# Optimization experiments

Hardware: AMD Instinct MI355X
Metric: run time of the kernel (lower is better)

The kernel has to match this reference:

```python
import jax, jax.numpy as jnp
import numpy as np

N = 49104   # anchors (from hardcoded [2, 49104, 80] in source)
C = 80      # classes
K = 100     # max detections kept per class (fixed for jit-able output shapes)
SCORE_THRESH = 0.05
IOU_THRESH = 0.5


def setup_inputs() -> dict:
    key = jax.random.key(0)
    k1, k2 = jax.random.split(key)
    scores = jax.random.uniform(k1, (N, C), dtype=jnp.float32)
    # build valid xyxy boxes inside an ~800x800 image
    r = jax.random.uniform(k2, (N, 4), dtype=jnp.float32)
    x1 = r[:, 0] * 768.0
    y1 = r[:, 1] * 768.0
    w = r[:, 2] * 96.0 + 4.0
    h = r[:, 3] * 96.0 + 4.0
    boxes = jnp.stack([x1, y1, x1 + w, y1 + h], axis=1)
    return {"scores": scores, "boxes": boxes}


def _nms_all(scores, boxes):
    """Per-class greedy NMS, vectorized over classes via vmap.
    scores: [N, C], boxes: [N, 4] xyxy. Returns idxs/scs/valid each [C, K]."""
    areas = (boxes[:, 2] - boxes[:, 0]) * (boxes[:, 3] - boxes[:, 1])  # [N]

    def iou_vs_all(b, b_area):  # b: [4]
        ix1 = jnp.maximum(b[0], boxes[:, 0])
        iy1 = jnp.maximum(b[1], boxes[:, 1])
        ix2 = jnp.minimum(b[2], boxes[:, 2])
        iy2 = jnp.minimum(b[3], boxes[:, 3])
        inter = jnp.clip(ix2 - ix1, 0.0) * jnp.clip(iy2 - iy1, 0.0)
        return inter / (b_area + areas - inter + 1e-8)  # [N]

    def nms_one_class(s_c):  # s_c: [N]
        # score threshold (matches `scores > 0.05` masking in the torch loop)
        s0 = jnp.where(s_c > SCORE_THRESH, s_c, -jnp.inf)

        def step(s, _):
            idx = jnp.argmax(s)
            sc = s[idx]
            keep = jnp.isfinite(sc)  # anything left above threshold?
            ious = iou_vs_all(boxes[idx], areas[idx])
            suppress = (ious > IOU_THRESH) & keep
            s_next = jnp.where(suppress, -jnp.inf, s).at[idx].set(-jnp.inf)
            return s_next, (idx, sc, keep)

        _, (idxs, scs, keeps) = jax.lax.scan(step, s0, None, length=K)
        return idxs, scs, keeps  # each [K]

    return jax.vmap(nms_one_class)(scores.T)  # map over C classes


def reference(scores, boxes):
    idxs, scs, valids = _nms_all(scores, boxes)  # [C, K] each
    idxs = idxs.reshape(-1)                       # [C*K]
    valids = valids.reshape(-1)                   # [C*K] bool
    final_scores = jnp.where(valids, scs.reshape(-1), 0.0)        # [C*K]
    final_classes = jnp.repeat(jnp.arange(C, dtype=jnp.int32), K)  # [C*K]
    final_boxes = boxes[idxs] * valids[:, None].astype(boxes.dtype)  # [C*K, 4]
    return final_scores, final_classes, final_boxes, valids
```

## Files before the change

### kernel.cpp

```cpp
#include <hip/hip_runtime.h>
#include <math.h>
#include <stdint.h>

#define N_ANCH 49104
#define NCLS 80
#define KDET 100
#define CAP 256
#define TPB 256
#define NBINS 1024
#define NBLK 512
#define SUBCAP 16
#define THETA 0.996090f
#define QTOT (N_ANCH * NCLS / 4)
#define JMAX 16
#define PADKEY(t) ((0xFFFFFFFFull << 16) | (uint64_t)(t))

#define LIST_ELEMS ((size_t)NCLS * NBLK * SUBCAP)
#define SUBCNT_OFF (LIST_ELEMS * 8)
#define WS_NEED (SUBCNT_OFF + (size_t)NCLS * NBLK * 4)

__device__ __forceinline__ void collect_quad(int q, float4 v, int* lcnt,
                                             uint64_t* __restrict__ list, int blk) {
    const int n = q / 20;
    const int c0 = 4 * (q % 20);
    float ss[4] = {v.x, v.y, v.z, v.w};
#pragma unroll
    for (int u = 0; u < 4; u++) {
        float s = ss[u];
        if (s > THETA) {
            int c = c0 + u;
            int p = atomicAdd(&lcnt[c], 1);
            if (p < SUBCAP) {
                uint32_t bits = __float_as_uint(s);
                list[((size_t)c * NBLK + blk) * SUBCAP + p] =
                    ((uint64_t)(~bits) << 16) | (uint64_t)n;
            }
        }
    }
}

__global__ __launch_bounds__(TPB) void collect_kernel(const float* __restrict__ scores,
                                                      uint64_t* __restrict__ list,
                                                      int* __restrict__ subcnt) {
    const int blk = blockIdx.x, tid = threadIdx.x;
    __shared__ int lcnt[NCLS];
    for (int c = tid; c < NCLS; c += TPB) lcnt[c] = 0;
    __syncthreads();
    const float4* sc4 = (const float4*)scores;
    const int stride = NBLK * TPB;
    int q = blk * TPB + tid;
    for (; q + 3 * stride < QTOT; q += 4 * stride) {
        float4 v0 = sc4[q], v1 = sc4[q + stride], v2 = sc4[q + 2 * stride], v3 = sc4[q + 3 * stride];
        collect_quad(q, v0, lcnt, list, blk);
        collect_quad(q + stride, v1, lcnt, list, blk);
        collect_quad(q + 2 * stride, v2, lcnt, list, blk);
        collect_quad(q + 3 * stride, v3, lcnt, list, blk);
    }
    for (; q < QTOT; q += stride) collect_quad(q, sc4[q], lcnt, list, blk);
    __syncthreads();
    for (int c = tid; c < NCLS; c += TPB) subcnt[c * NBLK + blk] = lcnt[c];
}

struct ChunkShared {
    uint64_t keys[CAP];
    float4   rbox[CAP];
    float    ra[CAP], rs[CAP];
    uint64_t smat[CAP * (CAP / 64)];
    uint64_t lwbuf[CAP / 64];
    uint64_t s_kw[CAP / 64];
    int      s_cw[4];
    float4   kbox[KDET];
    float    kar[KDET], ksc[KDET];
};

__device__ __forceinline__ int process_chunk(ChunkShared& S, int tid, int M, int kc0,
                                             const float* __restrict__ boxes) {
    if (M <= 0) return kc0;
    const int lane = tid & 63, wid = tid >> 6;
    const uint64_t key = S.keys[tid];
    const int n = (int)(key & 0xFFFFull);
    const int nc = n < N_ANCH ? n : N_ANCH - 1;
    const float4 mybox = *(const float4*)(boxes + (size_t)nc * 4);
    int rank = 0;
#pragma unroll 8
    for (int j = 0; j < CAP; j++) rank += (S.keys[j] < key) ? 1 : 0;
    S.rbox[rank] = mybox;
    S.ra[rank] = (mybox.z - mybox.x) * (mybox.w - mybox.y);
    S.rs[rank] = __uint_as_float(~((uint32_t)(key >> 16)));
    __syncthreads();
    bool alive = (tid < M);
    if (alive && kc0 > 0) {
        float4 b = S.rbox[tid];
        float arb = S.ra[tid];
        for (int k2 = 0; k2 < kc0; k2++) {
            float4 kb = S.kbox[k2];
            float ix1 = fmaxf(kb.x, b.x), iy1 = fmaxf(kb.y, b.y);
            float ix2 = fminf(kb.z, b.z), iy2 = fminf(kb.w, b.w);
            float inter = fmaxf(ix2 - ix1, 0.0f) * fmaxf(iy2 - iy1, 0.0f);
            float iou = inter / (S.kar[k2] + arb - inter + 1e-8f);
            if (iou > 0.5f) { alive = false; break; }
        }
    }
    {
        uint64_t bal = __ballot(alive);
        if (lane == 0) S.lwbuf[wid] = bal;
    }
    __syncthreads();
    for (int p = wid; p < 10; p += 4) {
        const int vw = (int)((0x3333222110ull >> (4 * p)) & 0xF);
        const int ws = (int)((0x3210210100ull >> (4 * p)) & 0xF);
        const int i0 = vw << 6;
        if (i0 >= M) continue;
        const int i1 = min(M, i0 + 64);
        const int jj = (ws << 6) + lane;
        float4 bj = S.rbox[jj];
        float arj = S.ra[jj];
        for (int i = i0; i < i1; i++) {
            bool bit = false;
            if (jj < i) {
                float4 bi = S.rbox[i];
                float ari = S.ra[i];
                float ix1 = fmaxf(bj.x, bi.x), iy1 = fmaxf(bj.y, bi.y);
                float ix2 = fminf(bj.z, bi.z), iy2 = fminf(bj.w, bi.w);
                float inter = fmaxf(ix2 - ix1, 0.0f) * fmaxf(iy2 - iy1, 0.0f);
                float iou = inter / (arj + ari - inter + 1e-8f);
                bit = iou > 0.5f;
            }
            uint64_t bb = __ballot(bit);
            if (lane == 0) S.smat[((size_t)i << 2) + ws] = bb;
        }
    }
    __syncthreads();
    uint64_t st0 = 0, st1 = 0, st2 = 0, st3 = 0;
    if (tid < M) {
        st0 = S.smat[((size_t)tid << 2) + 0];
        if (wid >= 1) st1 = S.smat[((size_t)tid << 2) + 1];
        if (wid >= 2) st2 = S.smat[((size_t)tid << 2) + 2];
        if (wid >= 3) st3 = S.smat[((size_t)tid << 2) + 3];
    }
    bool kept = alive;
    bool converged = false;
    for (int it = 0; it < JMAX; it++) {
        uint64_t kb = __ballot(kept);
        if (lane == 0) S.s_kw[wid] = kb;
        __syncthreads();
        const uint64_t k0 = S.s_kw[0], k1 = S.s_kw[1], k2 = S.s_kw[2], k3 = S.s_kw[3];
        const bool sup = ((k0 & st0) | (k1 & st1) | (k2 & st2) | (k3 & st3)) != 0ull;
        const bool nk = alive && !sup;
        uint64_t cb = __ballot(nk != kept);
        if (lane == 0) S.s_cw[wid] = (cb != 0ull) ? 1 : 0;
        kept = nk;
        __syncthreads();
        if ((S.s_cw[0] | S.s_cw[1] | S.s_cw[2] | S.s_cw[3]) == 0) { converged = true; break; }
    }
    if (!converged) {
        if (tid == 0) {
            uint64_t lv[4] = {S.lwbuf[0], S.lwbuf[1], S.lwbuf[2], S.lwbuf[3]};
            uint64_t kw[4] = {0, 0, 0, 0};
            for (int i = 0; i < M; i++) {
                const int w = i >> 6, b = i & 63;
                if (!((lv[w] >> b) & 1ull)) continue;
                const uint64_t* row = &S.smat[(size_t)i << 2];
                uint64_t sup = kw[0] & row[0];
                if (w >= 1) sup |= kw[1] & row[1];
                if (w >= 2) sup |= kw[2] & row[2];
                if (w >= 3) sup |= kw[3] & row[3];
                if (!sup) kw[w] |= 1ull << b;
            }
            S.s_kw[0] = kw[0]; S.s_kw[1] = kw[1]; S.s_kw[2] = kw[2]; S.s_kw[3] = kw[3];
        }
        __syncthreads();
    }
    const uint64_t k0 = S.s_kw[0], k1 = S.s_kw[1], k2 = S.s_kw[2], k3 = S.s_kw[3];
    const int total = __popcll(k0) + __popcll(k1) + __popcll(k2) + __popcll(k3);
    const uint64_t mykw = (wid == 0) ? k0 : (wid == 1) ? k1 : (wid == 2) ? k2 : k3;
    if (tid < M && ((mykw >> lane) & 1ull)) {
        int rk = __popcll(mykw & ((1ull << lane) - 1ull));
        if (wid > 0) rk += __popcll(k0);
        if (wid > 1) rk += __popcll(k1);
        if (wid > 2) rk += __popcll(k2);
        const int r = kc0 + rk;
        if (r < KDET) { S.kbox[r] = S.rbox[tid]; S.kar[r] = S.ra[tid]; S.ksc[r] = S.rs[tid]; }
    }
    __syncthreads();
    return min(kc0 + total, KDET);
}

__global__ __launch_bounds__(TPB) void nms_final(const float* __restrict__ scores,
                                                 const float* __restrict__ boxes,
                                                 const uint64_t* __restrict__ list,
                                                 const int* __restrict__ subcnt,
                                                 int use_lists,
                                                 float* __restrict__ out) {
    const int c = blockIdx.x, tid = threadIdx.x;
    const int lane = tid & 63, wid = tid >> 6;
    __shared__ ChunkShared S;
    __shared__ int hist[NBINS];
    __shared__ int s_wtot[4];
    __shared__ int s_ov, s_cnt, s_lo;

    int kc = 0;
    bool fast = false;
    if (use_lists) {
        const int raw0 = subcnt[c * NBLK + tid];
        const int raw1 = subcnt[c * NBLK + TPB + tid];
        S.keys[tid] = PADKEY(tid);
        if (tid == 0) s_ov = 0;
        __syncthreads();
        if (raw0 > SUBCAP || raw1 > SUBCAP) atomicOr(&s_ov, 1);
        const int v0 = min(raw0, SUBCAP), v1 = min(raw1, SUBCAP);
        const int v = v0 + v1;
        int incl = v;
        for (int d = 1; d < 64; d <<= 1) {
            int o = __shfl_up(incl, d, 64);
            if (lane >= d) incl += o;
        }
        if (lane == 63) s_wtot[wid] = incl;
        __syncthreads();
        int woff = 0;
        for (int w = 0; w < wid; w++) woff += s_wtot[w];
        const int off = woff + incl - v;
        const int M0 = s_wtot[0] + s_wtot[1] + s_wtot[2] + s_wtot[3];
        fast = (s_ov == 0) && (M0 <= CAP);
        if (fast && v > 0) {
            const uint64_t* src0 = list + ((size_t)c * NBLK + tid) * SUBCAP;
            const uint64_t* src1 = list + ((size_t)c * NBLK + TPB + tid) * SUBCAP;
            for (int k = 0; k < v0; k++) S.keys[off + k] = src0[k];
            for (int k = 0; k < v1; k++) S.keys[off + v0 + k] = src1[k];
        }
        __syncthreads();
        if (fast) kc = process_chunk(S, tid, M0, 0, boxes);
    }
    if (kc < KDET) {
        const float hicut = fast ? THETA : 3.0e38f;
        if (!fast) kc = 0;
        for (int b = tid; b < NBINS; b += TPB) hist[b] = 0;
        __syncthreads();
        for (int n = tid; n < N_ANCH; n += TPB) {
            float s = scores[(size_t)n * NCLS + c];
            if (s > 0.05f && s <= hicut) {
                int b = (int)(s * 1024.0f);
                b = b < 0 ? 0 : (b > NBINS - 1 ? NBINS - 1 : b);
                atomicAdd(&hist[b], 1);
            }
        }
        __syncthreads();
        int hi = NBINS;
        while (hi > 0 && kc < KDET) {
            if (tid == 0) {
                int lo = hi, tot = 0;
                while (lo > 0 && tot + hist[lo - 1] <= CAP) { lo--; tot += hist[lo]; }
                if (lo == hi) lo = hi - 1;
                s_lo = lo; s_cnt = 0;
            }
            S.keys[tid] = PADKEY(tid);
            __syncthreads();
            const int lo = s_lo;
            for (int n = tid; n < N_ANCH; n += TPB) {
                float s = scores[(size_t)n * NCLS + c];
                if (s > 0.05f && s <= hicut) {
                    int b = (int)(s * 1024.0f);
                    b = b < 0 ? 0 : (b > NBINS - 1 ? NBINS - 1 : b);
                    if (b >= lo && b < hi) {
                        int p = atomicAdd(&s_cnt, 1);
                        if (p < CAP) {
                            uint32_t bits = __float_as_uint(s);
                            S.keys[p] = ((uint64_t)(~bits) << 16) | (uint64_t)n;
                        }
                    }
                }
            }
            __syncthreads();
            const int M2 = min(s_cnt, CAP);
            kc = process_chunk(S, tid, M2, kc, boxes);
            hi = lo;
        }
    }
    __syncthreads();

    float* o_sc = out;
    float* o_cl = out + NCLS * KDET;
    float* o_bx = out + 2 * NCLS * KDET;
    float* o_va = out + 6 * NCLS * KDET;
    for (int k = tid; k < KDET; k += TPB) {
        bool valid = k < kc;
        o_sc[c * KDET + k] = valid ? S.ksc[k] : 0.0f;
        o_cl[c * KDET + k] = (float)c;
        o_va[c * KDET + k] = valid ? 1.0f : 0.0f;
        float4 bo;
        if (valid) bo = S.kbox[k];
        else { bo.x = 0.0f; bo.y = 0.0f; bo.z = 0.0f; bo.w = 0.0f; }
        *(float4*)(o_bx + ((size_t)(c * KDET + k)) * 4) = bo;
    }
}

extern "C" void kernel_launch(void* const* d_in, const int* in_sizes, int n_in,
                              void* d_out, int out_size, void* d_ws, size_t ws_size,
                              hipStream_t stream) {
    const float* scores = (const float*)d_in[0];
    const float* boxes  = (const float*)d_in[1];
    float* out = (float*)d_out;

    uint64_t* list   = (uint64_t*)d_ws;
    int*      subcnt = (int*)((char*)d_ws + SUBCNT_OFF);
    const int use_lists = (ws_size >= WS_NEED) ? 1 : 0;

    if (use_lists) {
        collect_kernel<<<NBLK, TPB, 0, stream>>>(scores, list, subcnt);
    }
    nms_final<<<NCLS, TPB, 0, stream>>>(scores, boxes, list, subcnt, use_lists, out);
}
```

Measured before the change: 100.0 us.

## Fuse collect and NMS into one cooperative kernel with a grid sync

Merges the candidate-collection kernel and the per-class NMS kernel into a single cooperative launch separated by a grid-wide barrier, and halves the collection grid to 256 blocks so every block can be co-resident. This removes one kernel launch and the inter-kernel gap. The cost is that collection now runs on fewer blocks, and the grid sync plus the larger shared-memory footprint per block may limit occupancy. A non-cooperative fallback kernel runs only the histogram slow path.

After: 154.2 us. +54.2%, slower.

```diff
diff --git a/kernel.cpp b/kernel.cpp
--- a/kernel.cpp
+++ b/kernel.cpp
@@ -1,6 +1,9 @@
 #include <hip/hip_runtime.h>
+#include <hip/hip_cooperative_groups.h>
 #include <math.h>
 #include <stdint.h>
+
+namespace cg = cooperative_groups;
 
 #define N_ANCH 49104
 #define NCLS 80
@@ -8,7 +11,7 @@
 #define CAP 256
 #define TPB 256
 #define NBINS 1024
-#define NBLK 512
+#define NBLK 256
 #define SUBCAP 16
 #define THETA 0.996090f
 #define QTOT (N_ANCH * NCLS / 4)
@@ -37,28 +40,6 @@
             }
         }
     }
-}
-
-__global__ __launch_bounds__(TPB) void collect_kernel(const float* __restrict__ scores,
-                                                      uint64_t* __restrict__ list,
-                                                      int* __restrict__ subcnt) {
-    const int blk = blockIdx.x, tid = threadIdx.x;
-    __shared__ int lcnt[NCLS];
-    for (int c = tid; c < NCLS; c += TPB) lcnt[c] = 0;
-    __syncthreads();
-    const float4* sc4 = (const float4*)scores;
-    const int stride = NBLK * TPB;
-    int q = blk * TPB + tid;
-    for (; q + 3 * stride < QTOT; q += 4 * stride) {
-        float4 v0 = sc4[q], v1 = sc4[q + stride], v2 = sc4[q + 2 * stride], v3 = sc4[q + 3 * stride];
-        collect_quad(q, v0, lcnt, list, blk);
-        collect_quad(q + stride, v1, lcnt, list, blk);
-        collect_quad(q + 2 * stride, v2, lcnt, list, blk);
-        collect_quad(q + 3 * stride, v3, lcnt, list, blk);
-    }
-    for (; q < QTOT; q += stride) collect_quad(q, sc4[q], lcnt, list, blk);
-    __syncthreads();
-    for (int c = tid; c < NCLS; c += TPB) subcnt[c * NBLK + blk] = lcnt[c];
 }
 
 struct ChunkShared {
@@ -186,98 +167,58 @@
     return min(kc0 + total, KDET);
 }
 
-__global__ __launch_bounds__(TPB) void nms_final(const float* __restrict__ scores,
-                                                 const float* __restrict__ boxes,
-                                                 const uint64_t* __restrict__ list,
-                                                 const int* __restrict__ subcnt,
-                                                 int use_lists,
-                                                 float* __restrict__ out) {
-    const int c = blockIdx.x, tid = threadIdx.x;
-    const int lane = tid & 63, wid = tid >> 6;
-    __shared__ ChunkShared S;
-    __shared__ int hist[NBINS];
-    __shared__ int s_wtot[4];
-    __shared__ int s_ov, s_cnt, s_lo;
-
-    int kc = 0;
-    bool fast = false;
-    if (use_lists) {
-        const int raw0 = subcnt[c * NBLK + tid];
-        const int raw1 = subcnt[c * NBLK + TPB + tid];
+__device__ __forceinline__ int slow_path(ChunkShared& S, int* hist, int* s_cnt, int* s_lo,
+                                         int c, int kc, bool fast, int tid,
+                                         const float* __restrict__ scores,
+                                         const float* __restrict__ boxes) {
+    const float hicut = fast ? THETA : 3.0e38f;
+    if (!fast) kc = 0;
+    for (int b = tid; b < NBINS; b += TPB) hist[b] = 0;
+    __syncthreads();
+    for (int n = tid; n < N_ANCH; n += TPB) {
+        float s = scores[(size_t)n * NCLS + c];
+        if (s > 0.05f && s <= hicut) {
+            int b = (int)(s * 1024.0f);
+            b = b < 0 ? 0 : (b > NBINS - 1 ? NBINS - 1 : b);
+            atomicAdd(&hist[b], 1);
+        }
+    }
+    __syncthreads();
+    int hi = NBINS;
+    while (hi > 0 && kc < KDET) {
+        if (tid == 0) {
+            int lo = hi, tot = 0;
+            while (lo > 0 && tot + hist[lo - 1] <= CAP) { lo--; tot += hist[lo]; }
+            if (lo == hi) lo = hi - 1;
+            *s_lo = lo; *s_cnt = 0;
+        }
         S.keys[tid] = PADKEY(tid);
-        if (tid == 0) s_ov = 0;
-        __syncthreads();
-        if (raw0 > SUBCAP || raw1 > SUBCAP) atomicOr(&s_ov, 1);
-        const int v0 = min(raw0, SUBCAP), v1 = min(raw1, SUBCAP);
-        const int v = v0 + v1;
-        int incl = v;
-        for (int d = 1; d < 64; d <<= 1) {
-            int o = __shfl_up(incl, d, 64);
-            if (lane >= d) incl += o;
-        }
-        if (lane == 63) s_wtot[wid] = incl;
-        __syncthreads();
-        int woff = 0;
-        for (int w = 0; w < wid; w++) woff += s_wtot[w];
-        const int off = woff + incl - v;
-        const int M0 = s_wtot[0] + s_wtot[1] + s_wtot[2] + s_wtot[3];
-        fast = (s_ov == 0) && (M0 <= CAP);
-        if (fast && v > 0) {
-            const uint64_t* src0 = list + ((size_t)c * NBLK + tid) * SUBCAP;
-            const uint64_t* src1 = list + ((size_t)c * NBLK + TPB + tid) * SUBCAP;
-            for (int k = 0; k < v0; k++) S.keys[off + k] = src0[k];
-            for (int k = 0; k < v1; k++) S.keys[off + v0 + k] = src1[k];
-        }
-        __syncthreads();
-        if (fast) kc = process_chunk(S, tid, M0, 0, boxes);
-    }
-    if (kc < KDET) {
-        const float hicut = fast ? THETA : 3.0e38f;
-        if (!fast) kc = 0;
-        for (int b = tid; b < NBINS; b += TPB) hist[b] = 0;
-        __syncthreads();
+        __syncthreads();
+        const int lo = *s_lo;
         for (int n = tid; n < N_ANCH; n += TPB) {
             float s = scores[(size_t)n * NCLS + c];
             if (s > 0.05f && s <= hicut) {
                 int b = (int)(s * 1024.0f);
                 b = b < 0 ? 0 : (b > NBINS - 1 ? NBINS - 1 : b);
-                atomicAdd(&hist[b], 1);
-            }
-        }
-        __syncthreads();
-        int hi = NBINS;
-        while (hi > 0 && kc < KDET) {
-            if (tid == 0) {
-                int lo = hi, tot = 0;
-                while (lo > 0 && tot + hist[lo - 1] <= CAP) { lo--; tot += hist[lo]; }
-                if (lo == hi) lo = hi - 1;
-                s_lo = lo; s_cnt = 0;
-            }
-            S.keys[tid] = PADKEY(tid);
-            __syncthreads();
-            const int lo = s_lo;
-            for (int n = tid; n < N_ANCH; n += TPB) {
-                float s = scores[(size_t)n * NCLS + c];
-                if (s > 0.05f && s <= hicut) {
-                    int b = (int)(s * 1024.0f);
-                    b = b < 0 ? 0 : (b > NBINS - 1 ? NBINS - 1 : b);
-                    if (b >= lo && b < hi) {
-                        int p = atomicAdd(&s_cnt, 1);
-                        if (p < CAP) {
-                            uint32_t bits = __float_as_uint(s);
-                            S.keys[p] = ((uint64_t)(~bits) << 16) | (uint64_t)n;
-                        }
+                if (b >= lo && b < hi) {
+                    int p = atomicAdd(s_cnt, 1);
+                    if (p < CAP) {
+                        uint32_t bits = __float_as_uint(s);
+                        S.keys[p] = ((uint64_t)(~bits) << 16) | (uint64_t)n;
                     }
                 }
             }
-            __syncthreads();
-            const int M2 = min(s_cnt, CAP);
-            kc = process_chunk(S, tid, M2, kc, boxes);
-            hi = lo;
-        }
-    }
-    __syncthreads();
-
+        }
+        __syncthreads();
+        const int M2 = min(*s_cnt, CAP);
+        kc = process_chunk(S, tid, M2, kc, boxes);
+        hi = lo;
+    }
+    return kc;
+}
+
+__device__ __forceinline__ void write_outputs(ChunkShared& S, int c, int kc, int tid,
+                                              float* __restrict__ out) {
     float* o_sc = out;
     float* o_cl = out + NCLS * KDET;
     float* o_bx = out + 2 * NCLS * KDET;
@@ -294,6 +235,88 @@
     }
 }
 
+__global__ __launch_bounds__(TPB) void nms_fused(const float* __restrict__ scores,
+                                                 const float* __restrict__ boxes,
+                                                 uint64_t* __restrict__ list,
+                                                 int* __restrict__ subcnt,
+                                                 float* __restrict__ out) {
+    const int blk = blockIdx.x, tid = threadIdx.x;
+    const int lane = tid & 63, wid = tid >> 6;
+    __shared__ ChunkShared S;
+    __shared__ int hist[NBINS];
+    __shared__ int lcnt[NCLS];
+    __shared__ int s_wtot[4];
+    __shared__ int s_ov, s_cnt, s_lo;
+
+    for (int cc = tid; cc < NCLS; cc += TPB) lcnt[cc] = 0;
+    __syncthreads();
+    {
+        const float4* sc4 = (const float4*)scores;
+        const int stride = NBLK * TPB;
+        int q = blk * TPB + tid;
+        for (; q + 3 * stride < QTOT; q += 4 * stride) {
+            float4 v0 = sc4[q], v1 = sc4[q + stride];
+            float4 v2 = sc4[q + 2 * stride], v3 = sc4[q + 3 * stride];
+            collect_quad(q, v0, lcnt, list, blk);
+            collect_quad(q + stride, v1, lcnt, list, blk);
+            collect_quad(q + 2 * stride, v2, lcnt, list, blk);
+            collect_quad(q + 3 * stride, v3, lcnt, list, blk);
+        }
+        for (; q < QTOT; q += stride) collect_quad(q, sc4[q], lcnt, list, blk);
+    }
+    __syncthreads();
+    for (int cc = tid; cc < NCLS; cc += TPB) subcnt[cc * NBLK + blk] = lcnt[cc];
+
+    __threadfence();
+    cg::this_grid().sync();
+    if (blk >= NCLS) return;
+
+    const int c = blk;
+    int kc = 0;
+    bool fast = false;
+    {
+        const int raw = subcnt[c * NBLK + tid];
+        S.keys[tid] = PADKEY(tid);
+        if (tid == 0) s_ov = 0;
+        __syncthreads();
+        if (raw > SUBCAP) atomicOr(&s_ov, 1);
+        const int v = min(raw, SUBCAP);
+        int incl = v;
+        for (int d = 1; d < 64; d <<= 1) {
+            int o = __shfl_up(incl, d, 64);
+            if (lane >= d) incl += o;
+        }
+        if (lane == 63) s_wtot[wid] = incl;
+        __syncthreads();
+        int woff = 0;
+        for (int w = 0; w < wid; w++) woff += s_wtot[w];
+        const int off = woff + incl - v;
+        const int M0 = s_wtot[0] + s_wtot[1] + s_wtot[2] + s_wtot[3];
+        fast = (s_ov == 0) && (M0 <= CAP);
+        if (fast && v > 0) {
+            const uint64_t* src = list + ((size_t)c * NBLK + tid) * SUBCAP;
+            for (int k = 0; k < v; k++) S.keys[off + k] = src[k];
+        }
+        __syncthreads();
+        if (fast) kc = process_chunk(S, tid, M0, 0, boxes);
+    }
+    if (kc < KDET) kc = slow_path(S, hist, &s_cnt, &s_lo, c, kc, fast, tid, scores, boxes);
+    __syncthreads();
+    write_outputs(S, c, kc, tid, out);
+}
+
+__global__ __launch_bounds__(TPB) void nms_slow(const float* __restrict__ scores,
+                                                const float* __restrict__ boxes,
+                                                float* __restrict__ out) {
+    const int c = blockIdx.x, tid = threadIdx.x;
+    __shared__ ChunkShared S;
+    __shared__ int hist[NBINS];
+    __shared__ int s_cnt, s_lo;
+    int kc = slow_path(S, hist, &s_cnt, &s_lo, c, 0, false, tid, scores, boxes);
+    __syncthreads();
+    write_outputs(S, c, kc, tid, out);
+}
+
 extern "C" void kernel_launch(void* const* d_in, const int* in_sizes, int n_in,
                               void* d_out, int out_size, void* d_ws, size_t ws_size,
                               hipStream_t stream) {
@@ -301,12 +324,18 @@
     const float* boxes  = (const float*)d_in[1];
     float* out = (float*)d_out;
 
-    uint64_t* list   = (uint64_t*)d_ws;
-    int*      subcnt = (int*)((char*)d_ws + SUBCNT_OFF);
-    const int use_lists = (ws_size >= WS_NEED) ? 1 : 0;
-
-    if (use_lists) {
-        collect_kernel<<<NBLK, TPB, 0, stream>>>(scores, list, subcnt);
-    }
-    nms_final<<<NCLS, TPB, 0, stream>>>(scores, boxes, list, subcnt, use_lists, out);
-}
+    if (ws_size >= WS_NEED) {
+        uint64_t* list   = (uint64_t*)d_ws;
+        int*      subcnt = (int*)((char*)d_ws + SUBCNT_OFF);
+        void* args[5];
+        args[0] = (void*)&scores;
+        args[1] = (void*)&boxes;
+        args[2] = (void*)&list;
+        args[3] = (void*)&subcnt;
+        args[4] = (void*)&out;
+        hipError_t e = hipLaunchCooperativeKernel((const void*)nms_fused, dim3(NBLK), dim3(TPB),
+                                                  args, 0, stream);
+        if (e == hipSuccess) return;
+    }
+    nms_slow<<<NCLS, TPB, 0, stream>>>(scores, boxes, out);
+}
```
